# Optimization experiments

Measured on AMD Instinct MI355X. Metric: run time of the kernel, lower is better.

Reference implementation:

```python
import jax, jax.numpy as jnp
import numpy as np

B, N, K = 2, 50000, 16
CIN, COUT, M = 64, 32, 4


def setup_inputs() -> dict:
    key = jax.random.key(0)
    ks = jax.random.split(key, 7)
    x = jax.random.normal(ks[0], (B, N, CIN), dtype=jnp.float32)
    adj = jax.random.randint(ks[1], (B, N, K), 0, N + 1)  # 0 == empty slot
    weight = jax.random.normal(ks[2], (M, COUT, CIN), dtype=jnp.float32) * 0.1
    bias = jax.random.normal(ks[3], (COUT,), dtype=jnp.float32) * 0.1
    u = jax.random.normal(ks[4], (M, CIN), dtype=jnp.float32) * 0.1
    v = jax.random.normal(ks[5], (M, CIN), dtype=jnp.float32) * 0.1
    c = jax.random.normal(ks[6], (M,), dtype=jnp.float32) * 0.1
    return {"x": x, "adj": adj, "weight": weight, "bias": bias,
            "u": u, "v": v, "c": c}


def _gather_padded(feat, adj):
    # feat: (B, N, ...); adj: (B, N, K) indices into zero-padded node axis
    # (index 0 selects the zero row, matching torch get_patches semantics)
    pad = jnp.zeros((feat.shape[0], 1) + feat.shape[2:], feat.dtype)
    feat_p = jnp.concatenate([pad, feat], axis=1)        # (B, N+1, ...)
    return jax.vmap(lambda f, a: f[a])(feat_p, adj)      # (B, N, K, ...)


def reference(x, adj, weight, bias, u, v, c):
    # degree normalization: 1/#nonzero-neighbors, 0 for isolated points
    deg = jnp.sum(adj != 0, axis=-1).astype(x.dtype)     # (B, N)
    inv_deg = jnp.where(deg != 0, 1.0 / deg, 0.0)        # (B, N)

    # mixture-kernel transform of every node, then neighbor gather
    wx = jnp.einsum('bnc,moc->bnmo', x, weight)          # (B, N, M, COUT)
    gathered = _gather_padded(wx, adj)                   # (B, N, K, M, COUT)

    # softmax-gated assignment q[b,n,k,m] = softmax_m(v.x_nbr + u.x_ctr + c)
    ux = jnp.einsum('mc,bnc->bnm', u, x)                 # (B, N, M)
    vx = jnp.einsum('mc,bnc->bnm', v, x)                 # (B, N, M)
    vg = _gather_padded(vx, adj)                         # (B, N, K, M)
    q = jax.nn.softmax(vg + ux[:, :, None, :] + c, axis=-1)

    # weighted sum over neighbors K and mixture components M
    out = jnp.einsum('bnkm,bnkmo->bno', q, gathered)     # (B, N, COUT)
    return out * inv_deg[..., None] + bias
```

## Files before the change

### kernel.cpp

```cpp
#include <hip/hip_runtime.h>

namespace {
constexpr int BB = 2;
constexpr int NN = 50000;
constexpr int KK = 16;
constexpr int CI = 64;
constexpr int CO = 32;
constexpr int MM = 4;
constexpr int BN = BB * NN;
constexpr int GROUPS = NN / 4;
constexpr int GRID = 768;
constexpr int WAVES = (GRID / 2) * 4;
}

typedef __attribute__((ext_vector_type(8))) short short8v;
typedef __attribute__((ext_vector_type(4))) float float4v;
typedef __attribute__((ext_vector_type(2))) float f32x2;

union F4P {
  float4 f4;
  f32x2 p[2];
};

__device__ __forceinline__ unsigned short bf16r(float f) {
  unsigned int u = __float_as_uint(f);
  u += 0x7FFFu + ((u >> 16) & 1u);
  return (unsigned short)(u >> 16);
}

__global__ __launch_bounds__(256) void k_prep(
    const float* __restrict__ x, const float* __restrict__ u,
    const float* __restrict__ v, float* __restrict__ ux,
    float* __restrict__ vx, unsigned short* __restrict__ xh) {
  int idx = blockIdx.x * 256 + threadIdx.x;
  if (idx >= BN) return;
  const float4* xr = (const float4*)(x + (size_t)idx * CI);
  float su[MM] = {0.f, 0.f, 0.f, 0.f};
  float sv[MM] = {0.f, 0.f, 0.f, 0.f};
  uint4 xpack[8];
#pragma unroll
  for (int t = 0; t < CI / 4; ++t) {
    float4 xv = xr[t];
#pragma unroll
    for (int m = 0; m < MM; ++m) {
      float4 uv = *(const float4*)(u + m * CI + t * 4);
      float4 vv = *(const float4*)(v + m * CI + t * 4);
      su[m] += uv.x * xv.x + uv.y * xv.y + uv.z * xv.z + uv.w * xv.w;
      sv[m] += vv.x * xv.x + vv.y * xv.y + vv.z * xv.z + vv.w * xv.w;
    }
    unsigned d0 = (unsigned)bf16r(xv.x) | ((unsigned)bf16r(xv.y) << 16);
    unsigned d1 = (unsigned)bf16r(xv.z) | ((unsigned)bf16r(xv.w) << 16);
    if (t & 1) {
      xpack[t >> 1].z = d0;
      xpack[t >> 1].w = d1;
    } else {
      xpack[t >> 1].x = d0;
      xpack[t >> 1].y = d1;
    }
  }
  ((float4*)ux)[idx] = make_float4(su[0], su[1], su[2], su[3]);
  ((float4*)vx)[idx] = make_float4(sv[0], sv[1], sv[2], sv[3]);
  uint4* xo = (uint4*)(xh + (size_t)idx * CI);
#pragma unroll
  for (int t = 0; t < 8; ++t) xo[t] = xpack[t];
}

__global__ __launch_bounds__(256, 3) void k_gather(
    const unsigned short* __restrict__ xh, const int* __restrict__ adj,
    const float* __restrict__ weight, const float* __restrict__ bias,
    const float* __restrict__ cvec, const float* __restrict__ ux,
    const float* __restrict__ vx, float* __restrict__ out) {
  __shared__ unsigned short w_lds[2 * 8 * 64 * 8];
  __shared__ unsigned short t_lds[4][8 * 256];
  __shared__ float q_lds[4][4][64];

  const int tid = threadIdx.x;
  const int lane = tid & 63;
  const int wv = tid >> 6;

  for (int i = tid; i < 2 * 8 * 64; i += 256) {
    int tl = i >> 9;
    int ks = (i >> 6) & 7;
    int l = i & 63;
    int o = tl * 16 + (l & 15);
    unsigned pk[4];
#pragma unroll
    for (int ee = 0; ee < 4; ++ee) {
      int k0 = ks * 32 + (l >> 4) * 8 + 2 * ee;
      unsigned lo = bf16r(weight[((k0 & 3) * CO + o) * CI + (k0 >> 2)]);
      unsigned hi =
          bf16r(weight[(((k0 + 1) & 3) * CO + o) * CI + ((k0 + 1) >> 2)]);
      pk[ee] = lo | (hi << 16);
    }
    *(uint4*)&w_lds[i * 8] = make_uint4(pk[0], pk[1], pk[2], pk[3]);
  }
  __syncthreads();

  const int m4 = lane & 3;
  const int k4 = lane >> 2;
  const float cm = cvec[m4];
  const float b0 = bias[lane & 15];
  const float b1 = bias[16 + (lane & 15)];

  const int xcd = blockIdx.x & 7;
  const int b = xcd >> 2;
  const int wb = ((blockIdx.x >> 3) << 2) | (xcd & 3);
  const int w = wb * 4 + wv;
  const size_t bbase = (size_t)b * NN;
  const unsigned short* xhb = xh + bbase * CI;
  const float* vxb = vx + bbase * MM;
  unsigned short* twv = t_lds[wv];

#define LOADS(n, GV)                                                       \
  _Pragma("unroll") for (int k = 0; k < KK; ++k) {                         \
    int r = __builtin_amdgcn_readlane(av_c, (n)*16 + k);                   \
    const unsigned short* rp = xhb + (size_t)(max(r, 1) - 1) * CI;         \
    GV[k] = rp[lane];                                                      \
  }

#define ACC_NODE(n, GV)                                                    \
  {                                                                        \
    const float4* qp = (const float4*)&q_lds[wv][n][0];                    \
    f32x2 t01 = {0.f, 0.f}, t23 = {0.f, 0.f};                              \
    _Pragma("unroll") for (int k = 0; k < KK; ++k) {                       \
      float xv = __uint_as_float(GV[k] << 16);                             \
      F4P qv;                                                              \
      qv.f4 = qp[k];                                                       \
      t01 += qv.p[0] * xv;                                                 \
      t23 += qv.p[1] * xv;                                                 \
    }                                                                      \
    unsigned lo, hi;                                                       \
    asm("v_cvt_pk_bf16_f32 %0, %1, %2"                                     \
        : "=v"(lo)                                                         \
        : "v"(t01[0]), "v"(t01[1]));                                       \
    asm("v_cvt_pk_bf16_f32 %0, %1, %2"                                     \
        : "=v"(hi)                                                         \
        : "v"(t23[0]), "v"(t23[1]));                                       \
    int row = jrows * 4 + (n);                                             \
    unsigned boff = (unsigned)row * 512u +                                 \
                    (((unsigned)lane * 8u) ^ ((unsigned)(row & 7) << 4));  \
    *(uint2*)((char*)twv + boff) = make_uint2(lo, hi);                     \
  }

#define FLUSH(JC)                                                          \
  {                                                                        \
    float4v ac0 = {0.f, 0.f, 0.f, 0.f};                                    \
    float4v ac1 = {0.f, 0.f, 0.f, 0.f};                                    \
    const int arow = lane & 7;                                             \
    const unsigned axor = (unsigned)(arow & 7) << 4;                       \
    _Pragma("unroll") for (int ks = 0; ks < 8; ++ks) {                     \
      unsigned aoff =                                                      \
          (unsigned)arow * 512u +                                          \
          ((((unsigned)(lane >> 4)) * 16u + (unsigned)ks * 64u) ^ axor);   \
      short8v A = *(const short8v*)((const char*)twv + aoff);              \
      short8v Bl = *(const short8v*)&w_lds[(0 * 8 + ks) * 512 + lane * 8]; \
      short8v Bh = *(const short8v*)&w_lds[(1 * 8 + ks) * 512 + lane * 8]; \
      ac0 = __builtin_amdgcn_mfma_f32_16x16x32_bf16(A, Bl, ac0, 0, 0, 0);  \
      ac1 = __builtin_amdgcn_mfma_f32_16x16x32_bf16(A, Bh, ac1, 0, 0, 0);  \
    }                                                                      \
    int jj = lane >> 4;                                                    \
    int gg = gbase + jj * WAVES;                                           \
    if (jj < (JC) && gg < GROUPS) {                                        \
      float* op = out + (bbase + (size_t)gg * 4) * CO + (lane & 15);       \
      op[0] = ac0[0] + b0;                                                 \
      op[16] = ac1[0] + b1;                                                \
      op[32] = ac0[1] + b0;                                                \
      op[48] = ac1[1] + b1;                                                \
      op[64] = ac0[2] + b0;                                                \
      op[80] = ac1[2] + b1;                                                \
      op[96] = ac0[3] + b0;                                                \
      op[112] = ac1[3] + b1;                                               \
    }                                                                      \
  }

  int g = w;
  int av = 0;
  if (g < GROUPS) av = adj[(bbase + (size_t)g * 4) * KK + lane];
  int jrows = 0;
  int gbase = g;

  while (g < GROUPS) {
    const int av_c = av;
    const size_t bn0 = bbase + (size_t)g * 4;

    int as0 = __shfl(av_c, k4);
    int as1 = __shfl(av_c, 16 + k4);
    int as2 = __shfl(av_c, 32 + k4);
    int as3 = __shfl(av_c, 48 + k4);
    float vg0 = vxb[(size_t)(max(as0, 1) - 1) * MM + m4];
    float vg1 = vxb[(size_t)(max(as1, 1) - 1) * MM + m4];
    float vg2 = vxb[(size_t)(max(as2, 1) - 1) * MM + m4];
    float vg3 = vxb[(size_t)(max(as3, 1) - 1) * MM + m4];
    float ux0 = ux[bn0 * MM + m4];
    float ux1 = ux[(bn0 + 1) * MM + m4];
    float ux2 = ux[(bn0 + 2) * MM + m4];
    float ux3 = ux[(bn0 + 3) * MM + m4];
    const unsigned long long msk = __ballot(av_c != 0);

    unsigned gv0[KK], gv1[KK], gv2[KK], gv3[KK];
    LOADS(0, gv0)
    LOADS(1, gv1)
    LOADS(2, gv2)
    LOADS(3, gv3)
    __builtin_amdgcn_sched_barrier(0);

    const int gn = g + WAVES;
    if (gn < GROUPS) av = adj[(bbase + (size_t)gn * 4) * KK + lane];

    {
      int d0 = __popc((unsigned)(msk & 0xFFFFull));
      int d1 = __popc((unsigned)((msk >> 16) & 0xFFFFull));
      int d2 = __popc((unsigned)((msk >> 32) & 0xFFFFull));
      int d3 = __popc((unsigned)((msk >> 48) & 0xFFFFull));
      float i0 = d0 ? __builtin_amdgcn_rcpf((float)d0) : 0.f;
      float i1 = d1 ? __builtin_amdgcn_rcpf((float)d1) : 0.f;
      float i2 = d2 ? __builtin_amdgcn_rcpf((float)d2) : 0.f;
      float i3 = d3 ? __builtin_amdgcn_rcpf((float)d3) : 0.f;
      float e0 = __expf(vg0 + ux0 + cm);
      float e1 = __expf(vg1 + ux1 + cm);
      float e2 = __expf(vg2 + ux2 + cm);
      float e3 = __expf(vg3 + ux3 + cm);
      float s0 = e0 + __shfl_xor(e0, 1);
      float s1 = e1 + __shfl_xor(e1, 1);
      float s2 = e2 + __shfl_xor(e2, 1);
      float s3 = e3 + __shfl_xor(e3, 1);
      s0 += __shfl_xor(s0, 2);
      s1 += __shfl_xor(s1, 2);
      s2 += __shfl_xor(s2, 2);
      s3 += __shfl_xor(s3, 2);
      q_lds[wv][0][lane] =
          (as0 != 0) ? e0 * __builtin_amdgcn_rcpf(s0) * i0 : 0.f;
      q_lds[wv][1][lane] =
          (as1 != 0) ? e1 * __builtin_amdgcn_rcpf(s1) * i1 : 0.f;
      q_lds[wv][2][lane] =
          (as2 != 0) ? e2 * __builtin_amdgcn_rcpf(s2) * i2 : 0.f;
      q_lds[wv][3][lane] =
          (as3 != 0) ? e3 * __builtin_amdgcn_rcpf(s3) * i3 : 0.f;
    }

    ACC_NODE(0, gv0)
    ACC_NODE(1, gv1)
    ACC_NODE(2, gv2)
    ACC_NODE(3, gv3)

    ++jrows;
    g = gn;
    if (jrows == 2) {
      FLUSH(2)
      jrows = 0;
      gbase = g;
    }
  }
  if (jrows > 0) FLUSH(jrows)
}

__global__ __launch_bounds__(256) void k_uxvx(
    const float* __restrict__ x, const float* __restrict__ u,
    const float* __restrict__ v, float* __restrict__ ux,
    float* __restrict__ vx) {
  int idx = blockIdx.x * 256 + threadIdx.x;
  if (idx >= BN) return;
  const float4* xr = (const float4*)(x + (size_t)idx * CI);
  float su[MM] = {0.f, 0.f, 0.f, 0.f};
  float sv[MM] = {0.f, 0.f, 0.f, 0.f};
#pragma unroll
  for (int t = 0; t < CI / 4; ++t) {
    float4 xv = xr[t];
#pragma unroll
    for (int m = 0; m < MM; ++m) {
      float4 uv = *(const float4*)(u + m * CI + t * 4);
      float4 vv = *(const float4*)(v + m * CI + t * 4);
      su[m] += uv.x * xv.x + uv.y * xv.y + uv.z * xv.z + uv.w * xv.w;
      sv[m] += vv.x * xv.x + vv.y * xv.y + vv.z * xv.z + vv.w * xv.w;
    }
  }
  ((float4*)ux)[idx] = make_float4(su[0], su[1], su[2], su[3]);
  ((float4*)vx)[idx] = make_float4(sv[0], sv[1], sv[2], sv[3]);
}

__global__ __launch_bounds__(256) void k_main_old(
    const float* __restrict__ x, const int* __restrict__ adj,
    const float* __restrict__ weight, const float* __restrict__ bias,
    const float* __restrict__ cvec, const float* __restrict__ ux,
    const float* __restrict__ vx, float* __restrict__ out) {
  __shared__ float w_lds2[MM][CO][CI + 4];
  __shared__ float q_lds2[4][64];
  __shared__ float t_lds2[4][MM][CI];
  const int tid = threadIdx.x;
  const int lane = tid & 63;
  const int wv = tid >> 6;
#pragma unroll
  for (int i = 0; i < (MM * CO * CI) / 256; ++i) {
    int g = i * 256 + tid;
    w_lds2[g >> 11][(g >> 6) & (CO - 1)][g & (CI - 1)] = weight[g];
  }
  __syncthreads();
  const int k4 = lane >> 2;
  const int m4 = lane & 3;
  const int o = lane & 31;
  const int hh = lane >> 5;
  const float cm = cvec[m4];
  const float bo = bias[o];
  for (int g = blockIdx.x; g < BN / 4; g += gridDim.x) {
    const int bn = g * 4 + wv;
    const int b = (bn >= NN) ? 1 : 0;
    const int* adjp = adj + (size_t)bn * KK;
    const float* xb = x + (size_t)b * NN * CI;
    int4 A[4];
#pragma unroll
    for (int i = 0; i < 4; ++i) A[i] = ((const int4*)adjp)[i];
    int deg = 0;
#pragma unroll
    for (int i = 0; i < 4; ++i)
      deg += (A[i].x != 0) + (A[i].y != 0) + (A[i].z != 0) + (A[i].w != 0);
    const float inv_deg = (deg > 0) ? 1.0f / (float)deg : 0.0f;
    int a = adjp[k4];
    float vg = 0.f;
    if (a != 0) vg = vx[((size_t)b * NN + (a - 1)) * MM + m4];
    float logit = vg + ux[(size_t)bn * MM + m4] + cm;
    float mx = fmaxf(logit, __shfl_xor(logit, 1));
    mx = fmaxf(mx, __shfl_xor(mx, 2));
    float e = __expf(logit - mx);
    float s = e + __shfl_xor(e, 1);
    s += __shfl_xor(s, 2);
    q_lds2[wv][lane] = (a != 0) ? (e / s) : 0.f;
    int rows[KK];
    {
      int tmp[KK] = {A[0].x, A[0].y, A[0].z, A[0].w, A[1].x, A[1].y,
                     A[1].z, A[1].w, A[2].x, A[2].y, A[2].z, A[2].w,
                     A[3].x, A[3].y, A[3].z, A[3].w};
#pragma unroll
      for (int k = 0; k < KK; ++k) rows[k] = max(tmp[k], 1) - 1;
    }
    float xg[KK];
#pragma unroll
    for (int k = 0; k < KK; ++k) xg[k] = xb[(size_t)rows[k] * CI + lane];
    float t0 = 0.f, t1 = 0.f, t2 = 0.f, t3 = 0.f;
#pragma unroll
    for (int k = 0; k < KK; ++k) {
      float4 qv = *(const float4*)&q_lds2[wv][k * 4];
      t0 += qv.x * xg[k];
      t1 += qv.y * xg[k];
      t2 += qv.z * xg[k];
      t3 += qv.w * xg[k];
    }
    t_lds2[wv][0][lane] = t0;
    t_lds2[wv][1][lane] = t1;
    t_lds2[wv][2][lane] = t2;
    t_lds2[wv][3][lane] = t3;
    float a0 = 0.f, a1 = 0.f, a2 = 0.f, a3 = 0.f;
#pragma unroll
    for (int mm = 0; mm < 2; ++mm) {
      const float* wrow = &w_lds2[2 * hh + mm][o][0];
      const float* trow = &t_lds2[wv][2 * hh + mm][0];
#pragma unroll
      for (int t4 = 0; t4 < CI / 4; ++t4) {
        float4 wvv = *(const float4*)(wrow + 4 * t4);
        float4 tv = *(const float4*)(trow + 4 * t4);
        a0 += wvv.x * tv.x;
        a1 += wvv.y * tv.y;
        a2 += wvv.z * tv.z;
        a3 += wvv.w * tv.w;
      }
    }
    float acc = (a0 + a1) + (a2 + a3);
    acc += __shfl_xor(acc, 32);
    if (lane < 32) out[(size_t)bn * CO + o] = acc * inv_deg + bo;
  }
}

extern "C" void kernel_launch(void* const* d_in, const int* in_sizes, int n_in,
                              void* d_out, int out_size, void* d_ws,
                              size_t ws_size, hipStream_t stream) {
  const float* x = (const float*)d_in[0];
  const int* adj = (const int*)d_in[1];
  const float* weight = (const float*)d_in[2];
  const float* bias = (const float*)d_in[3];
  const float* u = (const float*)d_in[4];
  const float* v = (const float*)d_in[5];
  const float* cvec = (const float*)d_in[6];
  float* out = (float*)d_out;

  float* ux = (float*)d_ws;
  float* vx = ux + (size_t)BN * MM;
  const size_t base = (size_t)BN * MM * 2 * sizeof(float);
  const size_t xh_bytes = (size_t)BN * CI * sizeof(unsigned short);

  if (ws_size >= base + xh_bytes) {
    unsigned short* xhb = (unsigned short*)((char*)d_ws + base);
    k_prep<<<(BN + 255) / 256, 256, 0, stream>>>(x, u, v, ux, vx, xhb);
    k_gather<<<GRID, 256, 0, stream>>>(xhb, adj, weight, bias, cvec, ux, vx,
                                       out);
  } else {
    k_uxvx<<<(BN + 255) / 256, 256, 0, stream>>>(x, u, v, ux, vx);
    k_main_old<<<1024, 256, 0, stream>>>(x, adj, weight, bias, cvec, ux, vx,
                                         out);
  }
}
```

Measured before the change: 66.44 us.

## Rewrite prep kernel with wave-tiled coalesced loads and MFMA for u/v projections

The per-node prep kernel is replaced by a version where each wave processes 16 nodes, loading x in coalesced chunks, writing the bf16 copy, and computing the u·x and v·x projections with bf16 MFMA instructions. This targets the poorly coalesced per-thread row reads and scalar dot-product work of the old prep pass. It lowers ux/vx precision from fp32 to bf16-input accumulation, which may change softmax gates slightly.

```diff
diff --git a/kernel.cpp b/kernel.cpp
--- a/kernel.cpp
+++ b/kernel.cpp
@@ -28,41 +28,73 @@
   return (unsigned short)(u >> 16);
 }
 
-__global__ __launch_bounds__(256) void k_prep(
+__global__ __launch_bounds__(256) void k_prep2(
     const float* __restrict__ x, const float* __restrict__ u,
     const float* __restrict__ v, float* __restrict__ ux,
     float* __restrict__ vx, unsigned short* __restrict__ xh) {
-  int idx = blockIdx.x * 256 + threadIdx.x;
-  if (idx >= BN) return;
-  const float4* xr = (const float4*)(x + (size_t)idx * CI);
-  float su[MM] = {0.f, 0.f, 0.f, 0.f};
-  float sv[MM] = {0.f, 0.f, 0.f, 0.f};
-  uint4 xpack[8];
-#pragma unroll
-  for (int t = 0; t < CI / 4; ++t) {
-    float4 xv = xr[t];
-#pragma unroll
-    for (int m = 0; m < MM; ++m) {
-      float4 uv = *(const float4*)(u + m * CI + t * 4);
-      float4 vv = *(const float4*)(v + m * CI + t * 4);
-      su[m] += uv.x * xv.x + uv.y * xv.y + uv.z * xv.z + uv.w * xv.w;
-      sv[m] += vv.x * xv.x + vv.y * xv.y + vv.z * xv.z + vv.w * xv.w;
-    }
-    unsigned d0 = (unsigned)bf16r(xv.x) | ((unsigned)bf16r(xv.y) << 16);
-    unsigned d1 = (unsigned)bf16r(xv.z) | ((unsigned)bf16r(xv.w) << 16);
-    if (t & 1) {
-      xpack[t >> 1].z = d0;
-      xpack[t >> 1].w = d1;
-    } else {
-      xpack[t >> 1].x = d0;
-      xpack[t >> 1].y = d1;
-    }
-  }
-  ((float4*)ux)[idx] = make_float4(su[0], su[1], su[2], su[3]);
-  ((float4*)vx)[idx] = make_float4(sv[0], sv[1], sv[2], sv[3]);
-  uint4* xo = (uint4*)(xh + (size_t)idx * CI);
-#pragma unroll
-  for (int t = 0; t < 8; ++t) xo[t] = xpack[t];
+  const int tid = threadIdx.x;
+  const int lane = tid & 63;
+  const int wv = tid >> 6;
+  const int col = lane & 15;
+  const int krow = lane >> 4;
+
+  short8v bfrag2[2];
+#pragma unroll
+  for (int ks = 0; ks < 2; ++ks)
+#pragma unroll
+    for (int e = 0; e < 8; ++e) {
+      int c = ks * 32 + krow * 8 + e;
+      float val = (col < 4) ? u[col * CI + c]
+                            : ((col < 8) ? v[(col - 4) * CI + c] : 0.f);
+      bfrag2[ks][e] = (short)bf16r(val);
+    }
+
+  const float4v zero = {0.f, 0.f, 0.f, 0.f};
+  const int nw = gridDim.x * 4;
+  for (int t = blockIdx.x * 4 + wv; t < BN / 16; t += nw) {
+    const int n0 = t * 16;
+    const float* xp = x + (size_t)(n0 + col) * CI + krow * 8;
+    short8v afrag[2];
+    uint4 hpack[2];
+#pragma unroll
+    for (int ks = 0; ks < 2; ++ks) {
+      float4 lo = *(const float4*)(xp + ks * 32);
+      float4 hi = *(const float4*)(xp + ks * 32 + 4);
+      unsigned short h0 = bf16r(lo.x), h1 = bf16r(lo.y);
+      unsigned short h2 = bf16r(lo.z), h3 = bf16r(lo.w);
+      unsigned short h4 = bf16r(hi.x), h5 = bf16r(hi.y);
+      unsigned short h6 = bf16r(hi.z), h7 = bf16r(hi.w);
+      afrag[ks][0] = (short)h0;
+      afrag[ks][1] = (short)h1;
+      afrag[ks][2] = (short)h2;
+      afrag[ks][3] = (short)h3;
+      afrag[ks][4] = (short)h4;
+      afrag[ks][5] = (short)h5;
+      afrag[ks][6] = (short)h6;
+      afrag[ks][7] = (short)h7;
+      hpack[ks] = make_uint4((unsigned)h0 | ((unsigned)h1 << 16),
+                             (unsigned)h2 | ((unsigned)h3 << 16),
+                             (unsigned)h4 | ((unsigned)h5 << 16),
+                             (unsigned)h6 | ((unsigned)h7 << 16));
+    }
+    unsigned short* xo = xh + (size_t)(n0 + col) * CI + krow * 8;
+    *(uint4*)(xo) = hpack[0];
+    *(uint4*)(xo + 32) = hpack[1];
+
+    float4v acc2 = zero;
+    acc2 = __builtin_amdgcn_mfma_f32_16x16x32_bf16(afrag[0], bfrag2[0], acc2,
+                                                   0, 0, 0);
+    acc2 = __builtin_amdgcn_mfma_f32_16x16x32_bf16(afrag[1], bfrag2[1], acc2,
+                                                   0, 0, 0);
+#pragma unroll
+    for (int ri = 0; ri < 4; ++ri) {
+      int node = n0 + krow * 4 + ri;
+      if (col < 4)
+        ux[(size_t)node * MM + col] = acc2[ri];
+      else if (col < 8)
+        vx[(size_t)node * MM + (col - 4)] = acc2[ri];
+    }
+  }
 }
 
 __global__ __launch_bounds__(256, 3) void k_gather(
@@ -388,7 +420,7 @@
 
   if (ws_size >= base + xh_bytes) {
     unsigned short* xhb = (unsigned short*)((char*)d_ws + base);
-    k_prep<<<(BN + 255) / 256, 256, 0, stream>>>(x, u, v, ux, vx, xhb);
+    k_prep2<<<1563, 256, 0, stream>>>(x, u, v, ux, vx, xhb);
     k_gather<<<GRID, 256, 0, stream>>>(xhb, adj, weight, bias, cvec, ux, vx,
                                        out);
   } else {
```

Result: faster. 62.53 us (median of 2 runs) (-5.9%).
